# Kernel optimization log

Measured on AMD Instinct MI355X. Metric: run time of the kernel, lower is better.

Reference implementation:

```python
import jax, jax.numpy as jnp
import numpy as np

HIDDEN = 128
N_HID = 7            # hidden_layers - 1 internal GELU blocks
N_TERMS = 2          # number of separable terms per side
N_IN = 1             # vars per term
B = 16384
STEP_SIZE = 0.1
NUM_STEPS = 1

# Forest-Ruth 4th-order symplectic coefficients
_K = 2.0 ** (1.0 / 3.0)
_C = (1.0 / (2.0 * (2.0 - _K)), (1.0 - _K) / (2.0 * (2.0 - _K)),
      (1.0 - _K) / (2.0 * (2.0 - _K)), 1.0 / (2.0 * (2.0 - _K)))
_D = (1.0 / (2.0 - _K), -_K / (2.0 - _K), 1.0 / (2.0 - _K), 0.0)


def _mlp(W0, b0, Wh, bh, Wo, bo, x):
    # x: [B, n_in] -> [B, 1]; torch GELU default is exact (erf)
    h = jax.nn.gelu(x @ W0 + b0, approximate=False)
    for i in range(N_HID):
        h = jax.nn.gelu(h @ Wh[i] + bh[i], approximate=False)
    return h @ Wo + bo


def _side_scalar(W0, b0, Wh, bh, Wo, bo, idx, x):
    # gather per-term feature subsets, run all term-MLPs batched via vmap,
    # sum over terms and batch (GradientWrapper takes grad of the summed scalar)
    xs = jnp.moveaxis(x[:, idx], 1, 0)            # [n_terms, B, n_in]
    outs = jax.vmap(_mlp)(W0, b0, Wh, bh, Wo, bo, xs)  # [n_terms, B, 1]
    return outs.sum()


def setup_inputs() -> dict:
    key = jax.random.key(0)
    ks = jax.random.split(key, 3)
    s = 0.05

    def pset(k):
        kk = jax.random.split(k, 6)
        return (
            jax.random.normal(kk[0], (N_TERMS, N_IN, HIDDEN), jnp.float32) * s,
            jax.random.normal(kk[1], (N_TERMS, HIDDEN), jnp.float32) * s,
            jax.random.normal(kk[2], (N_TERMS, N_HID, HIDDEN, HIDDEN), jnp.float32) * s,
            jax.random.normal(kk[3], (N_TERMS, N_HID, HIDDEN), jnp.float32) * s,
            jax.random.normal(kk[4], (N_TERMS, HIDDEN, 1), jnp.float32) * s,
            jax.random.normal(kk[5], (N_TERMS, 1), jnp.float32) * s,
        )

    lW0, lb0, lWh, lbh, lWo, lbo = pset(ks[0])
    rW0, rb0, rWh, rbh, rWo, rbo = pset(ks[1])
    X = jax.random.normal(ks[2], (B, 4), jnp.float32)
    left_idx = jnp.arange(N_TERMS, dtype=jnp.int32).reshape(N_TERMS, N_IN)
    right_idx = jnp.arange(N_TERMS, dtype=jnp.int32).reshape(N_TERMS, N_IN)
    return dict(X=X, lW0=lW0, lb0=lb0, lWh=lWh, lbh=lbh, lWo=lWo, lbo=lbo,
                rW0=rW0, rb0=rb0, rWh=rWh, rbh=rbh, rWo=rWo, rbo=rbo,
                left_idx=left_idx, right_idx=right_idx)


def reference(X, lW0, lb0, lWh, lbh, lWo, lbo,
              rW0, rb0, rWh, rbh, rWo, rbo, left_idx, right_idx):
    # H(q, p) = V(q) + T(p); left side = V(q), right side = T(p)
    dVdq = jax.grad(lambda q: _side_scalar(lW0, lb0, lWh, lbh, lWo, lbo, left_idx, q))
    dTdp = jax.grad(lambda p: _side_scalar(rW0, rb0, rWh, rbh, rWo, rbo, right_idx, p))
    dt = jnp.float32(STEP_SIZE)
    nq = X.shape[1] // 2
    q = X[:, :nq]
    p = X[:, nq:]
    for _ in range(NUM_STEPS):
        for c, d in zip(_C, _D):
            q = q + jnp.float32(c) * dt * dTdp(p)   # dq/dt =  dH/dp
            p = p - jnp.float32(d) * dt * dVdq(q)   # dp/dt = -dH/dq
    return jnp.concatenate((q, p), axis=1)
```

## Files before the change

### kernel.cpp

```cpp
#include <hip/hip_runtime.h>

#define NLAYER 7
#define IMGB 16384
#define WSCALE 16.0f

typedef __attribute__((ext_vector_type(2))) float float2v;
typedef __attribute__((ext_vector_type(4))) float float4v;
typedef __attribute__((ext_vector_type(2))) int   int2v;
typedef __attribute__((ext_vector_type(4))) int   int4v;
typedef __attribute__((ext_vector_type(4))) unsigned int uint4v;
typedef __attribute__((ext_vector_type(8))) int   int8v;
typedef unsigned long long u64;

__device__ __forceinline__ float2v pk_fma(float2v a, float2v b, float2v c){
  float2v d;
  asm("v_pk_fma_f32 %0, %1, %2, %3" : "=v"(d) : "v"(a), "v"(b), "v"(c));
  return d;
}
__device__ __forceinline__ float2v pk_mul(float2v a, float2v b){
  float2v d;
  asm("v_pk_mul_f32 %0, %1, %2" : "=v"(d) : "v"(a), "v"(b));
  return d;
}
__device__ __forceinline__ float2v pk_add(float2v a, float2v b){
  float2v d;
  asm("v_pk_add_f32 %0, %1, %2" : "=v"(d) : "v"(a), "v"(b));
  return d;
}
__device__ __forceinline__ float2v lo2(float4v v){ return (float2v){v[0], v[1]}; }
__device__ __forceinline__ float2v hi2(float4v v){ return (float2v){v[2], v[3]}; }

__device__ __forceinline__ unsigned pk4fp8(float v0, float v1, float v2, float v3){
  int w = __builtin_amdgcn_cvt_pk_fp8_f32(v0, v1, 0, false);
  w = __builtin_amdgcn_cvt_pk_fp8_f32(v2, v3, w, true);
  return (unsigned)w;
}
template<bool HI>
__device__ __forceinline__ float2v up2(unsigned w){
  return __builtin_amdgcn_cvt_pk_f32_fp8((int)w, HI);
}
__device__ __forceinline__ float4v mfma128(int8v a, int8v b){
  return __builtin_amdgcn_mfma_scale_f32_16x16x128_f8f6f4(
      a, b, (float4v){0.f,0.f,0.f,0.f}, 0, 0, 0, 0x7F7F7F7F, 0, 0x7F7F7F7F);
}
__device__ __forceinline__ void act2(float2v z, float2v& P16, float2v& gp16){
  const float2v c1v  = {6.3830764862829235f, 6.3830764862829235f};
  const float2v c3v  = {-1.0638460810704874f, -1.0638460810704874f};
  const float2v c33v = {-3.1915382432114624f, -3.1915382432114624f};
  const float2v v8   = {8.f, 8.f};
  float2v z2 = pk_mul(z, z);
  float2v u  = pk_fma(z2, c3v, c1v);
  P16 = pk_fma(z, u, v8);
  float2v Pd = pk_fma(z2, c33v, c1v);
  gp16 = pk_fma(z, Pd, P16);
}

__device__ __forceinline__ int8v ld_b(const unsigned char* row, int q, int m0){
  int2v x0 = *(const int2v*)(row + (((4*q+0) ^ m0)*8));
  int2v x1 = *(const int2v*)(row + (((4*q+1) ^ m0)*8));
  int2v x2 = *(const int2v*)(row + (((4*q+2) ^ m0)*8));
  int2v x3 = *(const int2v*)(row + (((4*q+3) ^ m0)*8));
  int4v lo = __builtin_shufflevector(x0, x1, 0, 1, 2, 3);
  int4v hi = __builtin_shufflevector(x2, x3, 0, 1, 2, 3);
  return __builtin_shufflevector(lo, hi, 0, 1, 2, 3, 4, 5, 6, 7);
}
__device__ __forceinline__ int8v ld_a(const unsigned char* p){
  int4v a0 = *(const int4v*)(p);
  int4v a1 = *(const int4v*)(p + 16);
  return __builtin_shufflevector(a0, a1, 0, 1, 2, 3, 4, 5, 6, 7);
}

__global__ __launch_bounds__(256)
void prep_weights(const float* __restrict__ lWh,
                  const float* __restrict__ rWh,
                  unsigned char* __restrict__ wbf)
{
  __shared__ __align__(16) unsigned char T[IMGB];
  const int b = blockIdx.x;
  const int net = b / NLAYER, L = b % NLAYER;
  const int side = net >> 1, term = net & 1;
  const float* src = (side ? rWh : lWh) + (size_t)((term*NLAYER + L)*128)*128;
  const int t = threadIdx.x;
  {
    const int k = t >> 1, n0 = (t & 1)*64;
    const float* row = src + k*128 + n0;
    #pragma unroll
    for (int c4 = 0; c4 < 4; ++c4){
      float4v f0 = *(const float4v*)(row + c4*16);
      float4v f1 = *(const float4v*)(row + c4*16 + 4);
      float4v f2 = *(const float4v*)(row + c4*16 + 8);
      float4v f3 = *(const float4v*)(row + c4*16 + 12);
      uint4v wv = { pk4fp8(f0[0]*WSCALE, f0[1]*WSCALE, f0[2]*WSCALE, f0[3]*WSCALE),
                    pk4fp8(f1[0]*WSCALE, f1[1]*WSCALE, f1[2]*WSCALE, f1[3]*WSCALE),
                    pk4fp8(f2[0]*WSCALE, f2[1]*WSCALE, f2[2]*WSCALE, f2[3]*WSCALE),
                    pk4fp8(f3[0]*WSCALE, f3[1]*WSCALE, f3[2]*WSCALE, f3[3]*WSCALE) };
      *(uint4v*)&T[k*128 + n0 + c4*16] = wv;
    }
  }
  __syncthreads();
  {
    const int n = t >> 1, c0 = (t & 1)*8;
    unsigned char* dst = wbf + ((size_t)b << 14) + n*128;
    #pragma unroll
    for (int c = 0; c < 8; ++c){
      const int kc = (c0 + c)*8;
      u64 v = 0;
      #pragma unroll
      for (int j = 0; j < 8; ++j)
        v |= (u64)T[(kc + j)*128 + n] << (8*j);
      *(u64*)(dst + (c0 + c)*8) = v;
    }
  }
}

__global__ __launch_bounds__(256, 4)
void sympl_main(const float* __restrict__ X,
                const float* __restrict__ lW0, const float* __restrict__ lb0,
                const float* __restrict__ lbh, const float* __restrict__ lWo,
                const float* __restrict__ rW0, const float* __restrict__ rb0,
                const float* __restrict__ rbh, const float* __restrict__ rWo,
                const int* __restrict__ lidx, const int* __restrict__ ridx,
                const unsigned char* __restrict__ wbf,
                float* __restrict__ out)
{
  __shared__ __align__(16) unsigned char sH[2][8192];

  const int tid  = threadIdx.x;
  const int lane = tid & 63;
  const int w    = tid >> 6;
  const int m0   = lane & 15;
  const int q    = lane >> 4;
  const int col  = blockIdx.y;
  const int e0   = blockIdx.x * 32;
  const int r    = tid >> 3;
  const int sg   = tid & 7;
  const int rs   = r & 15;

  const int lt = (lidx[0] == col) ? 0 : 1;
  const int rt = (ridx[0] == col) ? 0 : 1;

  float qv = X[(e0 + r)*4 + col];
  float pv = X[(e0 + r)*4 + 2 + col];

  const float dt = 0.1f;
  const float C0 = 0.6756035959798289f, C1 = -0.17560359597982883f;
  const float D0 = 1.3512071919596578f, D1 = -1.7024143839193153f;
  const float is = 1.0f / 262144.0f;
  const float coefs[7] = { C0*dt*is, -D0*dt*is, C1*dt*is, -D1*dt*is,
                           C1*dt*is, -D0*dt*is, C0*dt*is };

  const float2v K0 = {0.03125f, 0.03125f};
  const float2v K1 = {9.739801768e-5f, 9.739801768e-5f};
  const float2v K3 = {-2.476767495e-10f, -2.476767495e-10f};
  const float2v G0 = {0.125f, 0.125f};
  const float2v G1 = {7.791841414e-4f, 7.791841414e-4f};
  const float2v G3 = {-3.962875977e-9f, -3.962875977e-9f};
  const float2v v256p = {256.f, 256.f};

  const int aoff0 = ((2*w + 0)*16 + m0)*128 + q*32;
  const int aoff1 = ((2*w + 1)*16 + m0)*128 + q*32;

  int8v   pa0, pa1;
  float2v pbl0, pbh0, pbl1, pbh1;

  for (int ev = 0; ev < 7; ++ev){
    const bool isT = !(ev & 1);
    const int  term = isT ? rt : lt;
    const float* W0p = (isT ? rW0 : lW0) + term*128;
    const float* b0p = (isT ? rb0 : lb0) + term*128;
    const float* bhp = (isT ? rbh : lbh) + term*NLAYER*128;
    const float* Wop = (isT ? rWo : lWo) + term*128;
    const unsigned char* wimg = wbf + (size_t)(((isT ? 2 : 0) + term)*NLAYER)*IMGB;

    pa0 = ld_a(wimg + aoff0);
    pa1 = ld_a(wimg + aoff1);
    {
      float4v tb0 = *(const float4v*)(bhp + (2*w + 0)*16 + q*4);
      float4v tb1 = *(const float4v*)(bhp + (2*w + 1)*16 + q*4);
      pbl0 = pk_mul(lo2(tb0), v256p); pbh0 = pk_mul(hi2(tb0), v256p);
      pbl1 = pk_mul(lo2(tb1), v256p); pbh1 = pk_mul(hi2(tb1), v256p);
    }

    {
      const float x = isT ? pv : qv;
      const float2v xv = {x, x};
      unsigned char* pH = sH[0] + r*128;
      unsigned char* pD = pH + 4096;
      #pragma unroll
      for (int c = 0; c < 2; ++c){
        int n0 = sg*16 + c*8;
        float4v wa = *(const float4v*)(W0p + n0);
        float4v wb = *(const float4v*)(W0p + n0 + 4);
        float4v ba = *(const float4v*)(b0p + n0);
        float4v bb = *(const float4v*)(b0p + n0 + 4);
        float2v zp[4] = { pk_fma(xv, lo2(wa), lo2(ba)), pk_fma(xv, hi2(wa), hi2(ba)),
                          pk_fma(xv, lo2(wb), lo2(bb)), pk_fma(xv, hi2(wb), hi2(bb)) };
        float2v wp[4] = { lo2(wa), hi2(wa), lo2(wb), hi2(wb) };
        float Sh[8], Sd[8];
        #pragma unroll
        for (int pp = 0; pp < 4; ++pp){
          float2v P16, gp16; act2(zp[pp], P16, gp16);
          float2v h = pk_mul(zp[pp], P16);
          float2v d = pk_mul(gp16, wp[pp]);
          Sh[pp*2] = h[0]; Sh[pp*2+1] = h[1];
          Sd[pp*2] = d[0]; Sd[pp*2+1] = d[1];
        }
        u64 hv = (u64)pk4fp8(Sh[0],Sh[1],Sh[2],Sh[3]) | ((u64)pk4fp8(Sh[4],Sh[5],Sh[6],Sh[7]) << 32);
        u64 dv = (u64)pk4fp8(Sd[0],Sd[1],Sd[2],Sd[3]) | ((u64)pk4fp8(Sd[4],Sd[5],Sd[6],Sd[7]) << 32);
        int off = ((2*sg + c) ^ rs) * 8;
        *(u64*)(pH + off) = hv;
        *(u64*)(pD + off) = dv;
      }
    }
    __syncthreads();

    #pragma unroll
    for (int L = 0; L < NLAYER; ++L){
      const unsigned char* br = sH[L & 1] + m0*128;
      unsigned char* bw = sH[(L+1) & 1];

      int8v b00 = ld_b(br,        q, m0);
      int8v b01 = ld_b(br + 4096, q, m0);
      int8v b10 = ld_b(br + 2048, q, m0);
      int8v b11 = ld_b(br + 6144, q, m0);

      float4v acc[2][2][2];
      acc[0][0][0] = mfma128(pa0, b00);
      acc[0][0][1] = mfma128(pa0, b01);
      acc[0][1][0] = mfma128(pa0, b10);
      acc[0][1][1] = mfma128(pa0, b11);
      acc[1][0][0] = mfma128(pa1, b00);
      acc[1][0][1] = mfma128(pa1, b01);
      acc[1][1][0] = mfma128(pa1, b10);
      acc[1][1][1] = mfma128(pa1, b11);

      float2v bl0 = pbl0, bh0 = pbh0, bl1 = pbl1, bh1 = pbh1;

      if (L < NLAYER-1){
        const unsigned char* nimg = wimg + (size_t)(L+1)*IMGB;
        pa0 = ld_a(nimg + aoff0);
        pa1 = ld_a(nimg + aoff1);
        float4v tb0 = *(const float4v*)(bhp + (L+1)*128 + (2*w + 0)*16 + q*4);
        float4v tb1 = *(const float4v*)(bhp + (L+1)*128 + (2*w + 1)*16 + q*4);
        pbl0 = pk_mul(lo2(tb0), v256p); pbh0 = pk_mul(hi2(tb0), v256p);
        pbl1 = pk_mul(lo2(tb1), v256p); pbh1 = pk_mul(hi2(tb1), v256p);
      }

      const bool last = (L == NLAYER-1);
      #pragma unroll
      for (int t = 0; t < 2; ++t){
        const int I = 2*w + t;
        float2v bl = t ? bl1 : bl0;
        float2v bh = t ? bh1 : bh0;
        const int off = ((2*I + (q >> 1)) ^ m0) * 8 + (q & 1) * 4;
        #pragma unroll
        for (int gg = 0; gg < 2; ++gg){
          float2v ua = pk_add(lo2(acc[t][gg][0]), bl);
          float2v ub = pk_add(hi2(acc[t][gg][0]), bh);
          float2v u2a = pk_mul(ua, ua), u2b = pk_mul(ub, ub);
          float2v ga = pk_fma(ua, pk_fma(u2a, G3, G1), G0);
          float2v gb = pk_fma(ub, pk_fma(u2b, G3, G1), G0);
          float2v da = pk_mul(ga, lo2(acc[t][gg][1]));
          float2v db = pk_mul(gb, hi2(acc[t][gg][1]));
          unsigned char* base = bw + (gg*16 + m0)*128;
          if (!last){
            float2v ha = pk_mul(ua, pk_fma(ua, pk_fma(u2a, K3, K1), K0));
            float2v hb = pk_mul(ub, pk_fma(ub, pk_fma(u2b, K3, K1), K0));
            *(unsigned*)(base + off) = pk4fp8(ha[0], ha[1], hb[0], hb[1]);
          }
          *(unsigned*)(base + 4096 + off) = pk4fp8(da[0], da[1], db[0], db[1]);
        }
      }
      __syncthreads();
    }

    {
      const unsigned char* pD = sH[1] + 4096 + r*128;
      float2v sv = {0.f, 0.f};
      #pragma unroll
      for (int c = 0; c < 2; ++c){
        u64 dv8 = *(const u64*)(pD + ((2*sg + c) ^ rs) * 8);
        unsigned wlo = (unsigned)dv8, whi = (unsigned)(dv8 >> 32);
        float4v woa = *(const float4v*)(Wop + sg*16 + c*8);
        float4v wob = *(const float4v*)(Wop + sg*16 + c*8 + 4);
        sv = pk_fma(up2<false>(wlo), lo2(woa), sv);
        sv = pk_fma(up2<true>(wlo),  hi2(woa), sv);
        sv = pk_fma(up2<false>(whi), lo2(wob), sv);
        sv = pk_fma(up2<true>(whi),  hi2(wob), sv);
      }
      float s = sv[0] + sv[1];
      s += __shfl_xor(s, 1);
      s += __shfl_xor(s, 2);
      s += __shfl_xor(s, 4);
      if (isT) qv = fmaf(coefs[ev], s, qv);
      else     pv = fmaf(coefs[ev], s, pv);
    }
  }

  if (sg == 0){
    out[(e0 + r)*4 + col]     = qv;
    out[(e0 + r)*4 + 2 + col] = pv;
  }
}

extern "C" void kernel_launch(void* const* d_in, const int* in_sizes, int n_in,
                              void* d_out, int out_size, void* d_ws, size_t ws_size,
                              hipStream_t stream)
{
  const float* X   = (const float*)d_in[0];
  const float* lW0 = (const float*)d_in[1];
  const float* lb0 = (const float*)d_in[2];
  const float* lWh = (const float*)d_in[3];
  const float* lbh = (const float*)d_in[4];
  const float* lWo = (const float*)d_in[5];
  const float* rW0 = (const float*)d_in[7];
  const float* rb0 = (const float*)d_in[8];
  const float* rWh = (const float*)d_in[9];
  const float* rbh = (const float*)d_in[10];
  const float* rWo = (const float*)d_in[11];
  const int*   li  = (const int*)d_in[13];
  const int*   ri  = (const int*)d_in[14];
  unsigned char* wbf = (unsigned char*)d_ws;
  float* out = (float*)d_out;
  const int B = in_sizes[0] / 4;

  hipLaunchKernelGGL(prep_weights, dim3(4*NLAYER), dim3(256), 0, stream,
                     lWh, rWh, wbf);
  hipLaunchKernelGGL(sympl_main, dim3(B/32, 2), dim3(256), 0, stream,
                     X, lW0, lb0, lbh, lWo, rW0, rb0, rbh, rWo, li, ri, wbf, out);
}
```

Baseline: 215.0 us.

## Split batch tile into two halves and overlap MFMA with epilogue

Restructures the per-layer loop so the 32-row tile is split into two 16-row sub-tiles (A and B). The MFMAs of one sub-tile are issued while the GELU epilogue of the other runs, which is meant to hide MFMA latency behind VALU work. It also swaps inline-asm packed ops for compiler builtins so the scheduler can interleave them, and precomputes swizzled LDS pointers so accesses can use immediate offsets. In exchange it adds more live accumulators and register pressure, and the LDS layout is reorganised into a single 16 KB buffer.

```diff
diff --git a/kernel.cpp b/kernel.cpp
--- a/kernel.cpp
+++ b/kernel.cpp
@@ -12,20 +12,8 @@
 typedef __attribute__((ext_vector_type(8))) int   int8v;
 typedef unsigned long long u64;
 
-__device__ __forceinline__ float2v pk_fma(float2v a, float2v b, float2v c){
-  float2v d;
-  asm("v_pk_fma_f32 %0, %1, %2, %3" : "=v"(d) : "v"(a), "v"(b), "v"(c));
-  return d;
-}
-__device__ __forceinline__ float2v pk_mul(float2v a, float2v b){
-  float2v d;
-  asm("v_pk_mul_f32 %0, %1, %2" : "=v"(d) : "v"(a), "v"(b));
-  return d;
-}
-__device__ __forceinline__ float2v pk_add(float2v a, float2v b){
-  float2v d;
-  asm("v_pk_add_f32 %0, %1, %2" : "=v"(d) : "v"(a), "v"(b));
-  return d;
+__device__ __forceinline__ float2v f2fma(float2v a, float2v b, float2v c){
+  return __builtin_elementwise_fma(a, b, c);
 }
 __device__ __forceinline__ float2v lo2(float4v v){ return (float2v){v[0], v[1]}; }
 __device__ __forceinline__ float2v hi2(float4v v){ return (float2v){v[2], v[3]}; }
@@ -48,18 +36,20 @@
   const float2v c3v  = {-1.0638460810704874f, -1.0638460810704874f};
   const float2v c33v = {-3.1915382432114624f, -3.1915382432114624f};
   const float2v v8   = {8.f, 8.f};
-  float2v z2 = pk_mul(z, z);
-  float2v u  = pk_fma(z2, c3v, c1v);
-  P16 = pk_fma(z, u, v8);
-  float2v Pd = pk_fma(z2, c33v, c1v);
-  gp16 = pk_fma(z, Pd, P16);
-}
-
-__device__ __forceinline__ int8v ld_b(const unsigned char* row, int q, int m0){
-  int2v x0 = *(const int2v*)(row + (((4*q+0) ^ m0)*8));
-  int2v x1 = *(const int2v*)(row + (((4*q+1) ^ m0)*8));
-  int2v x2 = *(const int2v*)(row + (((4*q+2) ^ m0)*8));
-  int2v x3 = *(const int2v*)(row + (((4*q+3) ^ m0)*8));
+  float2v z2 = z * z;
+  float2v u  = f2fma(z2, c3v, c1v);
+  P16 = f2fma(z, u, v8);
+  float2v Pd = f2fma(z2, c33v, c1v);
+  gp16 = f2fma(z, Pd, P16);
+}
+
+__device__ __forceinline__ int8v ld_b(const unsigned char* r0, const unsigned char* r1,
+                                      const unsigned char* r2, const unsigned char* r3,
+                                      int imm){
+  int2v x0 = *(const int2v*)(r0 + imm);
+  int2v x1 = *(const int2v*)(r1 + imm);
+  int2v x2 = *(const int2v*)(r2 + imm);
+  int2v x3 = *(const int2v*)(r3 + imm);
   int4v lo = __builtin_shufflevector(x0, x1, 0, 1, 2, 3);
   int4v hi = __builtin_shufflevector(x2, x3, 0, 1, 2, 3);
   return __builtin_shufflevector(lo, hi, 0, 1, 2, 3, 4, 5, 6, 7);
@@ -123,7 +113,7 @@
                 const unsigned char* __restrict__ wbf,
                 float* __restrict__ out)
 {
-  __shared__ __align__(16) unsigned char sH[2][8192];
+  __shared__ __align__(16) unsigned char sH[16384];
 
   const int tid  = threadIdx.x;
   const int lane = tid & 63;
@@ -157,11 +147,42 @@
   const float2v G3 = {-3.962875977e-9f, -3.962875977e-9f};
   const float2v v256p = {256.f, 256.f};
 
+  const unsigned char* rp0 = sH + m0*128 + (((4*q+0) ^ m0)*8);
+  const unsigned char* rp1 = sH + m0*128 + (((4*q+1) ^ m0)*8);
+  const unsigned char* rp2 = sH + m0*128 + (((4*q+2) ^ m0)*8);
+  const unsigned char* rp3 = sH + m0*128 + (((4*q+3) ^ m0)*8);
+  unsigned char* wp0 = sH + m0*128 + (((2*(2*w+0) + (q>>1)) ^ m0)*8) + (q&1)*4;
+  unsigned char* wp1 = sH + m0*128 + (((2*(2*w+1) + (q>>1)) ^ m0)*8) + (q&1)*4;
+  unsigned char* l0w0 = sH + (r>>4)*8192 + rs*128 + (((2*sg+0) ^ rs)*8);
+  unsigned char* l0w1 = sH + (r>>4)*8192 + rs*128 + (((2*sg+1) ^ rs)*8);
+
   const int aoff0 = ((2*w + 0)*16 + m0)*128 + q*32;
   const int aoff1 = ((2*w + 1)*16 + m0)*128 + q*32;
 
   int8v   pa0, pa1;
   float2v pbl0, pbh0, pbl1, pbh1;
+
+#define MFMA_TILE(a00,a01,a10,a11, IMM) { \
+    int8v bh_ = ld_b(rp0,rp1,rp2,rp3, (IMM)); \
+    int8v bd_ = ld_b(rp0,rp1,rp2,rp3, (IMM)+2048); \
+    a00 = mfma128(pa0, bh_); a01 = mfma128(pa0, bd_); \
+    a10 = mfma128(pa1, bh_); a11 = mfma128(pa1, bd_); }
+
+#define EPI_HALF(aH,aD, BL,BH, WP, WIMM, LASTF) { \
+    float2v ua = lo2(aH) + (BL), ub = hi2(aH) + (BH); \
+    float2v u2a = ua*ua, u2b = ub*ub; \
+    float2v ga = f2fma(ua, f2fma(u2a, G3, G1), G0); \
+    float2v gb = f2fma(ub, f2fma(u2b, G3, G1), G0); \
+    float2v da = ga * lo2(aD), db = gb * hi2(aD); \
+    if (!(LASTF)){ \
+      float2v ha = ua * f2fma(ua, f2fma(u2a, K3, K1), K0); \
+      float2v hb = ub * f2fma(ub, f2fma(u2b, K3, K1), K0); \
+      *(unsigned*)((WP) + (WIMM)) = pk4fp8(ha[0], ha[1], hb[0], hb[1]); } \
+    *(unsigned*)((WP) + (WIMM) + 2048) = pk4fp8(da[0], da[1], db[0], db[1]); }
+
+#define EPI_TILE(a00,a01,a10,a11, WIMM, LASTF) { \
+    EPI_HALF(a00, a01, cbl0, cbh0, wp0, (WIMM), (LASTF)); \
+    EPI_HALF(a10, a11, cbl1, cbh1, wp1, (WIMM), (LASTF)); }
 
   for (int ev = 0; ev < 7; ++ev){
     const bool isT = !(ev & 1);
@@ -177,15 +198,13 @@
     {
       float4v tb0 = *(const float4v*)(bhp + (2*w + 0)*16 + q*4);
       float4v tb1 = *(const float4v*)(bhp + (2*w + 1)*16 + q*4);
-      pbl0 = pk_mul(lo2(tb0), v256p); pbh0 = pk_mul(hi2(tb0), v256p);
-      pbl1 = pk_mul(lo2(tb1), v256p); pbh1 = pk_mul(hi2(tb1), v256p);
+      pbl0 = lo2(tb0)*v256p; pbh0 = hi2(tb0)*v256p;
+      pbl1 = lo2(tb1)*v256p; pbh1 = hi2(tb1)*v256p;
     }
 
     {
       const float x = isT ? pv : qv;
       const float2v xv = {x, x};
-      unsigned char* pH = sH[0] + r*128;
-      unsigned char* pD = pH + 4096;
       #pragma unroll
       for (int c = 0; c < 2; ++c){
         int n0 = sg*16 + c*8;
@@ -193,100 +212,74 @@
         float4v wb = *(const float4v*)(W0p + n0 + 4);
         float4v ba = *(const float4v*)(b0p + n0);
         float4v bb = *(const float4v*)(b0p + n0 + 4);
-        float2v zp[4] = { pk_fma(xv, lo2(wa), lo2(ba)), pk_fma(xv, hi2(wa), hi2(ba)),
-                          pk_fma(xv, lo2(wb), lo2(bb)), pk_fma(xv, hi2(wb), hi2(bb)) };
-        float2v wp[4] = { lo2(wa), hi2(wa), lo2(wb), hi2(wb) };
+        float2v zp[4] = { f2fma(xv, lo2(wa), lo2(ba)), f2fma(xv, hi2(wa), hi2(ba)),
+                          f2fma(xv, lo2(wb), lo2(bb)), f2fma(xv, hi2(wb), hi2(bb)) };
+        float2v wpk[4] = { lo2(wa), hi2(wa), lo2(wb), hi2(wb) };
         float Sh[8], Sd[8];
         #pragma unroll
         for (int pp = 0; pp < 4; ++pp){
           float2v P16, gp16; act2(zp[pp], P16, gp16);
-          float2v h = pk_mul(zp[pp], P16);
-          float2v d = pk_mul(gp16, wp[pp]);
+          float2v h = zp[pp] * P16;
+          float2v d = gp16 * wpk[pp];
           Sh[pp*2] = h[0]; Sh[pp*2+1] = h[1];
           Sd[pp*2] = d[0]; Sd[pp*2+1] = d[1];
         }
-        u64 hv = (u64)pk4fp8(Sh[0],Sh[1],Sh[2],Sh[3]) | ((u64)pk4fp8(Sh[4],Sh[5],Sh[6],Sh[7]) << 32);
-        u64 dv = (u64)pk4fp8(Sd[0],Sd[1],Sd[2],Sd[3]) | ((u64)pk4fp8(Sd[4],Sd[5],Sd[6],Sd[7]) << 32);
-        int off = ((2*sg + c) ^ rs) * 8;
-        *(u64*)(pH + off) = hv;
-        *(u64*)(pD + off) = dv;
+        unsigned char* l0w = c ? l0w1 : l0w0;
+        *(unsigned*)(l0w)          = pk4fp8(Sh[0],Sh[1],Sh[2],Sh[3]);
+        *(unsigned*)(l0w + 4)      = pk4fp8(Sh[4],Sh[5],Sh[6],Sh[7]);
+        *(unsigned*)(l0w + 2048)   = pk4fp8(Sd[0],Sd[1],Sd[2],Sd[3]);
+        *(unsigned*)(l0w + 2052)   = pk4fp8(Sd[4],Sd[5],Sd[6],Sd[7]);
       }
     }
     __syncthreads();
+
+    float4v aA00, aA01, aA10, aA11;
+    float4v aB00, aB01, aB10, aB11;
+    float2v cbl0, cbh0, cbl1, cbh1;
+
+    MFMA_TILE(aA00, aA01, aA10, aA11, 0);
 
     #pragma unroll
     for (int L = 0; L < NLAYER; ++L){
-      const unsigned char* br = sH[L & 1] + m0*128;
-      unsigned char* bw = sH[(L+1) & 1];
-
-      int8v b00 = ld_b(br,        q, m0);
-      int8v b01 = ld_b(br + 4096, q, m0);
-      int8v b10 = ld_b(br + 2048, q, m0);
-      int8v b11 = ld_b(br + 6144, q, m0);
-
-      float4v acc[2][2][2];
-      acc[0][0][0] = mfma128(pa0, b00);
-      acc[0][0][1] = mfma128(pa0, b01);
-      acc[0][1][0] = mfma128(pa0, b10);
-      acc[0][1][1] = mfma128(pa0, b11);
-      acc[1][0][0] = mfma128(pa1, b00);
-      acc[1][0][1] = mfma128(pa1, b01);
-      acc[1][1][0] = mfma128(pa1, b10);
-      acc[1][1][1] = mfma128(pa1, b11);
-
-      float2v bl0 = pbl0, bh0 = pbh0, bl1 = pbl1, bh1 = pbh1;
-
+      const int cb_ = (L & 1) * 4096;
+      const int nb  = ((L+1) & 1) * 4096;
+      const bool last = (L == NLAYER-1);
+
+      cbl0 = pbl0; cbh0 = pbh0; cbl1 = pbl1; cbh1 = pbh1;
+
+      EPI_TILE(aA00, aA01, aA10, aA11, nb, last);
+      MFMA_TILE(aB00, aB01, aB10, aB11, 8192 + cb_);
       if (L < NLAYER-1){
         const unsigned char* nimg = wimg + (size_t)(L+1)*IMGB;
         pa0 = ld_a(nimg + aoff0);
         pa1 = ld_a(nimg + aoff1);
         float4v tb0 = *(const float4v*)(bhp + (L+1)*128 + (2*w + 0)*16 + q*4);
         float4v tb1 = *(const float4v*)(bhp + (L+1)*128 + (2*w + 1)*16 + q*4);
-        pbl0 = pk_mul(lo2(tb0), v256p); pbh0 = pk_mul(hi2(tb0), v256p);
-        pbl1 = pk_mul(lo2(tb1), v256p); pbh1 = pk_mul(hi2(tb1), v256p);
-      }
-
-      const bool last = (L == NLAYER-1);
-      #pragma unroll
-      for (int t = 0; t < 2; ++t){
-        const int I = 2*w + t;
-        float2v bl = t ? bl1 : bl0;
-        float2v bh = t ? bh1 : bh0;
-        const int off = ((2*I + (q >> 1)) ^ m0) * 8 + (q & 1) * 4;
-        #pragma unroll
-        for (int gg = 0; gg < 2; ++gg){
-          float2v ua = pk_add(lo2(acc[t][gg][0]), bl);
-          float2v ub = pk_add(hi2(acc[t][gg][0]), bh);
-          float2v u2a = pk_mul(ua, ua), u2b = pk_mul(ub, ub);
-          float2v ga = pk_fma(ua, pk_fma(u2a, G3, G1), G0);
-          float2v gb = pk_fma(ub, pk_fma(u2b, G3, G1), G0);
-          float2v da = pk_mul(ga, lo2(acc[t][gg][1]));
-          float2v db = pk_mul(gb, hi2(acc[t][gg][1]));
-          unsigned char* base = bw + (gg*16 + m0)*128;
-          if (!last){
-            float2v ha = pk_mul(ua, pk_fma(ua, pk_fma(u2a, K3, K1), K0));
-            float2v hb = pk_mul(ub, pk_fma(ub, pk_fma(u2b, K3, K1), K0));
-            *(unsigned*)(base + off) = pk4fp8(ha[0], ha[1], hb[0], hb[1]);
-          }
-          *(unsigned*)(base + 4096 + off) = pk4fp8(da[0], da[1], db[0], db[1]);
-        }
+        pbl0 = lo2(tb0)*v256p; pbh0 = hi2(tb0)*v256p;
+        pbl1 = lo2(tb1)*v256p; pbh1 = hi2(tb1)*v256p;
       }
       __syncthreads();
+
+      EPI_TILE(aB00, aB01, aB10, aB11, 8192 + nb, last);
+      if (L < NLAYER-1){
+        MFMA_TILE(aA00, aA01, aA10, aA11, nb);
+      }
+      __syncthreads();
     }
 
     {
-      const unsigned char* pD = sH[1] + 4096 + r*128;
       float2v sv = {0.f, 0.f};
       #pragma unroll
       for (int c = 0; c < 2; ++c){
-        u64 dv8 = *(const u64*)(pD + ((2*sg + c) ^ rs) * 8);
+        const unsigned char* l0w = c ? l0w1 : l0w0;
+        u64 dv8 = *(const u64*)(l0w + 4096 + 2048);
         unsigned wlo = (unsigned)dv8, whi = (unsigned)(dv8 >> 32);
         float4v woa = *(const float4v*)(Wop + sg*16 + c*8);
         float4v wob = *(const float4v*)(Wop + sg*16 + c*8 + 4);
-        sv = pk_fma(up2<false>(wlo), lo2(woa), sv);
-        sv = pk_fma(up2<true>(wlo),  hi2(woa), sv);
-        sv = pk_fma(up2<false>(whi), lo2(wob), sv);
-        sv = pk_fma(up2<true>(whi),  hi2(wob), sv);
+        sv = f2fma(up2<false>(wlo), lo2(woa), sv);
+        sv = f2fma(up2<true>(wlo),  hi2(woa), sv);
+        sv = f2fma(up2<false>(whi), lo2(wob), sv);
+        sv = f2fma(up2<true>(whi),  hi2(wob), sv);
       }
       float s = sv[0] + sv[1];
       s += __shfl_xor(s, 1);
@@ -301,6 +294,9 @@
     out[(e0 + r)*4 + col]     = qv;
     out[(e0 + r)*4 + 2 + col] = pv;
   }
+#undef MFMA_TILE
+#undef EPI_HALF
+#undef EPI_TILE
 }
 
 extern "C" void kernel_launch(void* const* d_in, const int* in_sizes, int n_in,
```

Result: faster. 206.8 us (-3.8%).
